# Performance work log

Measured on AMD Instinct MI355X. Metric: run time of the kernel, lower is better.

The kernel has to match this reference:

```python
import jax, jax.numpy as jnp
import numpy as np

B, S, SIZE = 2048, 512, 96  # size = embedding_size(32) * num_feature(3)


def setup_inputs() -> dict:
    key = jax.random.key(0)
    k1, k2, k3, k4, k5, k6, k7 = jax.random.split(key, 7)
    bound = 1.0 / np.sqrt(SIZE)  # nn.Linear default init range
    return {
        "seq_item_embedding": jax.random.normal(k1, (B, S, SIZE), dtype=jnp.float32),
        "target_item_embedding": jax.random.normal(k2, (B, 1, SIZE), dtype=jnp.float32),
        "mask": jax.random.randint(k3, (B, S + 1, 1), 0, 2).astype(jnp.bool_),
        "w1_weight": jax.random.uniform(k4, (SIZE, SIZE), jnp.float32, -bound, bound),
        "w1_bias": jax.random.uniform(k5, (SIZE,), jnp.float32, -bound, bound),
        "w2_weight": jax.random.uniform(k6, (SIZE, SIZE), jnp.float32, -bound, bound),
        "w2_bias": jax.random.uniform(k7, (SIZE,), jnp.float32, -bound, bound),
    }


def reference(seq_item_embedding, target_item_embedding, mask,
              w1_weight, w1_bias, w2_weight, w2_bias):
    # mask[:, :-1, :] -> [B, S] boolean (True = masked out)
    m = mask[:, :-1, 0]
    # w1(seq): [B, S, size]; note source reassigns seq_item_embedding to this,
    # so the final weighted pool uses the projected sequence.
    seq_h = jnp.einsum('bsd,ed->bse', seq_item_embedding, w1_weight) + w1_bias
    # w2(target): [B, 1, size], broadcasts over seq_len (repeat in torch)
    tgt_h = jnp.einsum('bqd,ed->bqe', target_item_embedding, w2_weight) + w2_bias
    # sigmoid(sum) reduced over feature dim -> scores [B, S]
    scores = jax.nn.sigmoid(seq_h + tgt_h).sum(axis=-1)
    scores = jnp.where(m, jnp.float32(-1e9), scores)
    attn = jax.nn.softmax(scores, axis=-1)  # [B, S]
    # weighted pool over seq dim -> [B, size]
    output = jnp.einsum('bs,bse->be', attn, seq_h)
    return output
```

## Files before the change

kernel.cpp:

```cpp
#include <hip/hip_runtime.h>
#include <math.h>

#define NB 2048
#define NS 512
#define ND 96

typedef __attribute__((ext_vector_type(8))) short short8;
typedef __attribute__((ext_vector_type(4))) float floatx4;

__device__ __forceinline__ unsigned f2bfu(float f) {
    union { float f; unsigned u; } c; c.f = f;
    unsigned u = c.u;
    u += 0x7FFF + ((u >> 16) & 1);
    return u >> 16;
}
__device__ __forceinline__ unsigned pack2(float a, float b) {
    return f2bfu(a) | (f2bfu(b) << 16);
}
__device__ __forceinline__ float lo_f(unsigned u) {
    union { unsigned u; float f; } c; c.u = u << 16; return c.f;
}
__device__ __forceinline__ float hi_f(unsigned u) {
    union { unsigned u; float f; } c; c.u = u & 0xFFFF0000u; return c.f;
}
__device__ __forceinline__ float sigm(float x) {
    return 1.0f / (1.0f + __expf(-x));
}

__global__ __launch_bounds__(512, 4)
void attn_fused(const float* __restrict__ seq,
                const float* __restrict__ tgt,
                const int*   __restrict__ mask,
                const float* __restrict__ w1,
                const float* __restrict__ b1,
                const float* __restrict__ w2,
                const float* __restrict__ b2,
                float* __restrict__ out)
{
    __shared__ short w1f[18 * 64 * 8];
    __shared__ float sc[NS];
    __shared__ float at[NS];
    __shared__ float th[ND];
    __shared__ float red1[8], red2[8];
    __shared__ float osum[8][ND];

    const int b    = blockIdx.x;
    const int tid  = threadIdx.x;
    const int lane = tid & 63;
    const int wave = tid >> 6;
    const int l15  = lane & 15;
    const int quad = lane >> 4;

    for (int idx = tid; idx < 1152; idx += 512) {
        const int e  = idx / 12;
        const int dc = idx - 12 * e;
        const int kk = dc >> 2;
        const int q  = dc & 3;
        const float* p = w1 + e * ND + kk * 32 + q * 8;
        floatx4 p0 = *(const floatx4*)(p);
        floatx4 p1 = *(const floatx4*)(p + 4);
        short8 v;
        v[0]=(short)f2bfu(p0[0]); v[1]=(short)f2bfu(p0[1]);
        v[2]=(short)f2bfu(p0[2]); v[3]=(short)f2bfu(p0[3]);
        v[4]=(short)f2bfu(p1[0]); v[5]=(short)f2bfu(p1[1]);
        v[6]=(short)f2bfu(p1[2]); v[7]=(short)f2bfu(p1[3]);
        const int t = e >> 4, r = e & 15;
        *(short8*)&w1f[(((t * 3 + kk) * 64) + q * 16 + r) * 8] = v;
    }

    if (tid < ND) {
        const float* tv = tgt + (size_t)b * ND;
        const float* wr = w2 + tid * ND;
        float acc = b2[tid];
        #pragma unroll
        for (int d = 0; d < ND; d += 4) {
            acc += tv[d]*wr[d] + tv[d+1]*wr[d+1] + tv[d+2]*wr[d+2] + tv[d+3]*wr[d+3];
        }
        th[tid] = acc;
    }
    __syncthreads();

    float tgtv[6], biasv[6];
    #pragma unroll
    for (int t = 0; t < 6; ++t) {
        tgtv[t]  = th[16 * t + l15];
        biasv[t] = b1[16 * t + l15];
    }

    unsigned pk[4][6][2];
    const float* abase = seq + ((size_t)b * NS + l15) * ND + quad * 8;

    #pragma unroll
    for (int sti = 0; sti < 4; ++sti) {
        const int s0 = (wave * 4 + sti) * 16;
        short8 af[3];
        #pragma unroll
        for (int kk = 0; kk < 3; ++kk) {
            const float* p = abase + (size_t)s0 * ND + kk * 32;
            floatx4 p0 = *(const floatx4*)(p);
            floatx4 p1 = *(const floatx4*)(p + 4);
            short8 v;
            v[0]=(short)f2bfu(p0[0]); v[1]=(short)f2bfu(p0[1]);
            v[2]=(short)f2bfu(p0[2]); v[3]=(short)f2bfu(p0[3]);
            v[4]=(short)f2bfu(p1[0]); v[5]=(short)f2bfu(p1[1]);
            v[6]=(short)f2bfu(p1[2]); v[7]=(short)f2bfu(p1[3]);
            af[kk] = v;
        }
        float p0s = 0.f, p1s = 0.f, p2s = 0.f, p3s = 0.f;
        #pragma unroll
        for (int t = 0; t < 6; ++t) {
            floatx4 acc = { biasv[t], biasv[t], biasv[t], biasv[t] };
            #pragma unroll
            for (int kk = 0; kk < 3; ++kk) {
                const short8 bf = *(const short8*)&w1f[((t * 3 + kk) * 64 + lane) * 8];
                acc = __builtin_amdgcn_mfma_f32_16x16x32_bf16(af[kk], bf, acc, 0, 0, 0);
            }
            pk[sti][t][0] = pack2(acc[0], acc[1]);
            pk[sti][t][1] = pack2(acc[2], acc[3]);
            const float thv = tgtv[t];
            p0s += sigm(acc[0] + thv);
            p1s += sigm(acc[1] + thv);
            p2s += sigm(acc[2] + thv);
            p3s += sigm(acc[3] + thv);
        }
        #pragma unroll
        for (int off = 1; off < 16; off <<= 1) {
            p0s += __shfl_xor(p0s, off, 64);
            p1s += __shfl_xor(p1s, off, 64);
            p2s += __shfl_xor(p2s, off, 64);
            p3s += __shfl_xor(p3s, off, 64);
        }
        if (l15 == 0) {
            sc[s0 + quad * 4 + 0] = p0s;
            sc[s0 + quad * 4 + 1] = p1s;
            sc[s0 + quad * 4 + 2] = p2s;
            sc[s0 + quad * 4 + 3] = p3s;
        }
    }
    __syncthreads();

    float v = sc[tid];
    if (mask[(size_t)b * (NS + 1) + tid] != 0) v = -1e9f;
    float mx = v;
    #pragma unroll
    for (int off = 1; off < 64; off <<= 1) mx = fmaxf(mx, __shfl_xor(mx, off, 64));
    if (lane == 0) red1[wave] = mx;
    __syncthreads();
    mx = red1[0];
    #pragma unroll
    for (int w = 1; w < 8; ++w) mx = fmaxf(mx, red1[w]);
    const float e0 = __expf(v - mx);
    float ssum = e0;
    #pragma unroll
    for (int off = 1; off < 64; off <<= 1) ssum += __shfl_xor(ssum, off, 64);
    if (lane == 0) red2[wave] = ssum;
    __syncthreads();
    float tot = red2[0];
    #pragma unroll
    for (int w = 1; w < 8; ++w) tot += red2[w];
    at[tid] = e0 * (1.0f / tot);
    __syncthreads();

    float o[6] = {0.f, 0.f, 0.f, 0.f, 0.f, 0.f};
    #pragma unroll
    for (int sti = 0; sti < 4; ++sti) {
        const int s0 = (wave * 4 + sti) * 16 + quad * 4;
        const float a0 = at[s0], a1 = at[s0 + 1], a2 = at[s0 + 2], a3 = at[s0 + 3];
        #pragma unroll
        for (int t = 0; t < 6; ++t) {
            const unsigned u0 = pk[sti][t][0];
            const unsigned u1 = pk[sti][t][1];
            o[t] += a0 * lo_f(u0) + a1 * hi_f(u0) + a2 * lo_f(u1) + a3 * hi_f(u1);
        }
    }
    #pragma unroll
    for (int t = 0; t < 6; ++t) {
        o[t] += __shfl_xor(o[t], 16, 64);
        o[t] += __shfl_xor(o[t], 32, 64);
    }
    if (quad == 0) {
        #pragma unroll
        for (int t = 0; t < 6; ++t) osum[wave][16 * t + l15] = o[t];
    }
    __syncthreads();
    if (tid < ND) {
        float a = 0.f;
        #pragma unroll
        for (int w = 0; w < 8; ++w) a += osum[w][tid];
        out[(size_t)b * ND + tid] = a;
    }
}

extern "C" void kernel_launch(void* const* d_in, const int* in_sizes, int n_in,
                              void* d_out, int out_size, void* d_ws, size_t ws_size,
                              hipStream_t stream) {
    const float* seq  = (const float*)d_in[0];
    const float* tgt  = (const float*)d_in[1];
    const int*   mask = (const int*)d_in[2];
    const float* w1   = (const float*)d_in[3];
    const float* b1   = (const float*)d_in[4];
    const float* w2   = (const float*)d_in[5];
    const float* b2   = (const float*)d_in[6];
    float* out = (float*)d_out;
    attn_fused<<<dim3(NB), dim3(512), 0, stream>>>(seq, tgt, mask, w1, b1, w2, b2, out);
}
```

Baseline: 591.8 us.

## Drop softmax max pass, keep scores in registers, prefetch first seq tile

Each sequence score is a sum of 96 sigmoids, so it lies in [0, 96]. The softmax therefore subtracts the constant 96 instead of a block-wide max, which removes one reduction and its barriers. Scores and attention weights now move between lanes with shuffles instead of shared arrays, which removes two more __syncthreads. The first seq tile is loaded before the weight staging starts, and the target matvec is split across 4 threads with vector loads. In exchange, a row whose positions are all masked now gives 0/0 instead of uniform weights, and small scores may underflow exp.

```diff
diff --git a/kernel.cpp b/kernel.cpp
--- a/kernel.cpp
+++ b/kernel.cpp
@@ -25,6 +25,14 @@
 }
 __device__ __forceinline__ float sigm(float x) {
     return 1.0f / (1.0f + __expf(-x));
+}
+__device__ __forceinline__ short8 cvt8(floatx4 p0, floatx4 p1) {
+    short8 v;
+    v[0]=(short)f2bfu(p0[0]); v[1]=(short)f2bfu(p0[1]);
+    v[2]=(short)f2bfu(p0[2]); v[3]=(short)f2bfu(p0[3]);
+    v[4]=(short)f2bfu(p1[0]); v[5]=(short)f2bfu(p1[1]);
+    v[6]=(short)f2bfu(p1[2]); v[7]=(short)f2bfu(p1[3]);
+    return v;
 }
 
 __global__ __launch_bounds__(512, 4)
@@ -38,10 +46,8 @@
                 float* __restrict__ out)
 {
     __shared__ short w1f[18 * 64 * 8];
-    __shared__ float sc[NS];
-    __shared__ float at[NS];
-    __shared__ float th[ND];
-    __shared__ float red1[8], red2[8];
+    __shared__ floatx4 thp4[ND];
+    __shared__ float red2[8];
     __shared__ float osum[8][ND];
 
     const int b    = blockIdx.x;
@@ -50,6 +56,19 @@
     const int wave = tid >> 6;
     const int l15  = lane & 15;
     const int quad = lane >> 4;
+
+    const int m = mask[(size_t)b * (NS + 1) + tid];
+    const float* abase = seq + ((size_t)b * NS + l15) * ND + quad * 8;
+
+    floatx4 pre[6];
+    {
+        const float* p = abase + (size_t)(wave * 64) * ND;
+        #pragma unroll
+        for (int kk = 0; kk < 3; ++kk) {
+            pre[2 * kk]     = *(const floatx4*)(p + kk * 32);
+            pre[2 * kk + 1] = *(const floatx4*)(p + kk * 32 + 4);
+        }
+    }
 
     for (int idx = tid; idx < 1152; idx += 512) {
         const int e  = idx / 12;
@@ -59,52 +78,52 @@
         const float* p = w1 + e * ND + kk * 32 + q * 8;
         floatx4 p0 = *(const floatx4*)(p);
         floatx4 p1 = *(const floatx4*)(p + 4);
-        short8 v;
-        v[0]=(short)f2bfu(p0[0]); v[1]=(short)f2bfu(p0[1]);
-        v[2]=(short)f2bfu(p0[2]); v[3]=(short)f2bfu(p0[3]);
-        v[4]=(short)f2bfu(p1[0]); v[5]=(short)f2bfu(p1[1]);
-        v[6]=(short)f2bfu(p1[2]); v[7]=(short)f2bfu(p1[3]);
         const int t = e >> 4, r = e & 15;
-        *(short8*)&w1f[(((t * 3 + kk) * 64) + q * 16 + r) * 8] = v;
-    }
-
-    if (tid < ND) {
-        const float* tv = tgt + (size_t)b * ND;
-        const float* wr = w2 + tid * ND;
-        float acc = b2[tid];
-        #pragma unroll
-        for (int d = 0; d < ND; d += 4) {
-            acc += tv[d]*wr[d] + tv[d+1]*wr[d+1] + tv[d+2]*wr[d+2] + tv[d+3]*wr[d+3];
-        }
-        th[tid] = acc;
+        *(short8*)&w1f[(((t * 3 + kk) * 64) + q * 16 + r) * 8] = cvt8(p0, p1);
+    }
+
+    if (tid < 4 * ND) {
+        const int e    = tid >> 2;
+        const int part = tid & 3;
+        const float* tv = tgt + (size_t)b * ND + part * 24;
+        const float* wr = w2 + e * ND + part * 24;
+        float acc = 0.f;
+        #pragma unroll
+        for (int d = 0; d < 24; d += 4) {
+            floatx4 a = *(const floatx4*)(tv + d);
+            floatx4 w = *(const floatx4*)(wr + d);
+            acc += a[0]*w[0] + a[1]*w[1] + a[2]*w[2] + a[3]*w[3];
+        }
+        thp4[e][part] = acc;
     }
     __syncthreads();
 
     float tgtv[6], biasv[6];
     #pragma unroll
     for (int t = 0; t < 6; ++t) {
-        tgtv[t]  = th[16 * t + l15];
-        biasv[t] = b1[16 * t + l15];
+        const int e = 16 * t + l15;
+        floatx4 tp = thp4[e];
+        tgtv[t]  = b2[e] + tp[0] + tp[1] + tp[2] + tp[3];
+        biasv[t] = b1[e];
     }
 
     unsigned pk[4][6][2];
-    const float* abase = seq + ((size_t)b * NS + l15) * ND + quad * 8;
+    float myscore = 0.f;
 
     #pragma unroll
     for (int sti = 0; sti < 4; ++sti) {
         const int s0 = (wave * 4 + sti) * 16;
         short8 af[3];
-        #pragma unroll
-        for (int kk = 0; kk < 3; ++kk) {
-            const float* p = abase + (size_t)s0 * ND + kk * 32;
-            floatx4 p0 = *(const floatx4*)(p);
-            floatx4 p1 = *(const floatx4*)(p + 4);
-            short8 v;
-            v[0]=(short)f2bfu(p0[0]); v[1]=(short)f2bfu(p0[1]);
-            v[2]=(short)f2bfu(p0[2]); v[3]=(short)f2bfu(p0[3]);
-            v[4]=(short)f2bfu(p1[0]); v[5]=(short)f2bfu(p1[1]);
-            v[6]=(short)f2bfu(p1[2]); v[7]=(short)f2bfu(p1[3]);
-            af[kk] = v;
+        if (sti == 0) {
+            af[0] = cvt8(pre[0], pre[1]);
+            af[1] = cvt8(pre[2], pre[3]);
+            af[2] = cvt8(pre[4], pre[5]);
+        } else {
+            #pragma unroll
+            for (int kk = 0; kk < 3; ++kk) {
+                const float* p = abase + (size_t)s0 * ND + kk * 32;
+                af[kk] = cvt8(*(const floatx4*)(p), *(const floatx4*)(p + 4));
+            }
         }
         float p0s = 0.f, p1s = 0.f, p2s = 0.f, p3s = 0.f;
         #pragma unroll
@@ -130,26 +149,16 @@
             p2s += __shfl_xor(p2s, off, 64);
             p3s += __shfl_xor(p3s, off, 64);
         }
-        if (l15 == 0) {
-            sc[s0 + quad * 4 + 0] = p0s;
-            sc[s0 + quad * 4 + 1] = p1s;
-            sc[s0 + quad * 4 + 2] = p2s;
-            sc[s0 + quad * 4 + 3] = p3s;
-        }
-    }
-    __syncthreads();
-
-    float v = sc[tid];
-    if (mask[(size_t)b * (NS + 1) + tid] != 0) v = -1e9f;
-    float mx = v;
-    #pragma unroll
-    for (int off = 1; off < 64; off <<= 1) mx = fmaxf(mx, __shfl_xor(mx, off, 64));
-    if (lane == 0) red1[wave] = mx;
-    __syncthreads();
-    mx = red1[0];
-    #pragma unroll
-    for (int w = 1; w < 8; ++w) mx = fmaxf(mx, red1[w]);
-    const float e0 = __expf(v - mx);
+        float pv = p0s;
+        pv = ((lane & 3) == 1) ? p1s : pv;
+        pv = ((lane & 3) == 2) ? p2s : pv;
+        pv = ((lane & 3) == 3) ? p3s : pv;
+        const int src = (((lane >> 2) & 3) << 4) | (lane & 3);
+        const float g = __shfl(pv, src, 64);
+        if ((lane >> 4) == sti) myscore = g;
+    }
+
+    float e0 = (m != 0) ? 0.0f : __expf(myscore - 96.0f);
     float ssum = e0;
     #pragma unroll
     for (int off = 1; off < 64; off <<= 1) ssum += __shfl_xor(ssum, off, 64);
@@ -158,14 +167,16 @@
     float tot = red2[0];
     #pragma unroll
     for (int w = 1; w < 8; ++w) tot += red2[w];
-    at[tid] = e0 * (1.0f / tot);
-    __syncthreads();
+    const float atv = e0 * (1.0f / tot);
 
     float o[6] = {0.f, 0.f, 0.f, 0.f, 0.f, 0.f};
     #pragma unroll
     for (int sti = 0; sti < 4; ++sti) {
-        const int s0 = (wave * 4 + sti) * 16 + quad * 4;
-        const float a0 = at[s0], a1 = at[s0 + 1], a2 = at[s0 + 2], a3 = at[s0 + 3];
+        const int sb = sti * 16 + quad * 4;
+        const float a0 = __shfl(atv, sb + 0, 64);
+        const float a1 = __shfl(atv, sb + 1, 64);
+        const float a2 = __shfl(atv, sb + 2, 64);
+        const float a3 = __shfl(atv, sb + 3, 64);
         #pragma unroll
         for (int t = 0; t < 6; ++t) {
             const unsigned u0 = pk[sti][t][0];
```

Measured after the change: 718.6 us. +21.4%, slower.
